# Kernel tuning notes

Measured on AMD Instinct MI355X. Metric: run time of the kernel, lower is better.

The kernel has to match this reference:

```python
import jax, jax.numpy as jnp
import numpy as np
import math

B, N, D, H, L, F, K = 4, 256, 768, 32, 12, 3072, 128
HD = D // H
ATOM_TYPES = 64
EDGE_TYPES = ATOM_TYPES * ATOM_TYPES
BLOCKS = 1
SQRT_2PI = math.sqrt(2.0 * math.pi)


def _ln(x, g, b):
    m = jnp.mean(x, -1, keepdims=True)
    v = jnp.mean((x - m) ** 2, -1, keepdims=True)
    return (x - m) * jax.lax.rsqrt(v + 1e-5) * g + b


def _gelu(x):
    return jax.nn.gelu(x, approximate=False)


def setup_inputs():
    key = jax.random.key(0)
    ks = iter(jax.random.split(key, 64))
    def nrm(shape, s=0.02):
        return jax.random.normal(next(ks), shape, jnp.float32) * s
    inp = dict(
        atoms=jax.random.randint(next(ks), (B, N), 0, ATOM_TYPES),
        tags=jax.random.randint(next(ks), (B, N), 0, 3),
        pos=jax.random.normal(next(ks), (B, N, 3), jnp.float32) * 3.0,
        real_mask=jnp.ones((B, N), dtype=bool),
        atom_emb=nrm((ATOM_TYPES, D)),
        tag_emb=nrm((3, D)),
        gbf_means=jax.random.uniform(next(ks), (K,), jnp.float32, 0.0, 3.0),
        gbf_stds=jax.random.uniform(next(ks), (K,), jnp.float32, 0.0, 3.0),
        gbf_mul=jnp.ones((EDGE_TYPES, 1), jnp.float32),
        gbf_bias=jnp.zeros((EDGE_TYPES, 1), jnp.float32),
        bp_w1=nrm((K, K)), bp_b1=jnp.zeros((K,), jnp.float32),
        bp_w2=nrm((H, K)), bp_b2=jnp.zeros((H,), jnp.float32),
        ep_w=nrm((D, K)), ep_b=jnp.zeros((D,), jnp.float32),
        ln1_g=jnp.ones((L, D), jnp.float32), ln1_b=jnp.zeros((L, D), jnp.float32),
        wqkv=nrm((L, 3 * D, D)), bqkv=jnp.zeros((L, 3 * D), jnp.float32),
        wo=nrm((L, D, D)), bo=jnp.zeros((L, D), jnp.float32),
        ln2_g=jnp.ones((L, D), jnp.float32), ln2_b=jnp.zeros((L, D), jnp.float32),
        w1=nrm((L, F, D)), b1=jnp.zeros((L, F), jnp.float32),
        w2=nrm((L, D, F)), b2=jnp.zeros((L, D), jnp.float32),
        fln_g=jnp.ones((D,), jnp.float32), fln_b=jnp.zeros((D,), jnp.float32),
        en_w1=nrm((D, D)), en_b1=jnp.zeros((D,), jnp.float32),
        en_w2=nrm((1, D)), en_b2=jnp.zeros((1,), jnp.float32),
        eagg=nrm((3, 1), 0.01),
        nq_w=nrm((D, D)), nq_b=jnp.zeros((D,), jnp.float32),
        nk_w=nrm((D, D)), nk_b=jnp.zeros((D,), jnp.float32),
        nv_w=nrm((D, D)), nv_b=jnp.zeros((D,), jnp.float32),
        f1_w=nrm((1, D)), f1_b=jnp.zeros((1,), jnp.float32),
        f2_w=nrm((1, D)), f2_b=jnp.zeros((1,), jnp.float32),
        f3_w=nrm((1, D)), f3_b=jnp.zeros((1,), jnp.float32),
    )
    return inp


def _forward(atoms, tags, real_mask, pos, atom_emb, tag_emb, gbf_means, gbf_stds, gbf_mul, gbf_bias,
             bp_w1, bp_b1, bp_w2, bp_b2, ep_w, ep_b,
             ln1_g, ln1_b, wqkv, bqkv, wo, bo, ln2_g, ln2_b, w1, b1, w2, b2,
             fln_g, fln_b, en_w1, en_b1, en_w2, en_b2, eagg,
             nq_w, nq_b, nk_w, nk_b, nv_w, nv_b, f1_w, f1_b, f2_w, f2_b, f3_w, f3_b):
    pad = atoms == 0                                              # [B,N]
    # delta[b,i,j] = pos[b,j] - pos[b,i]  (matches pos.unsqueeze(1) - pos.unsqueeze(2))
    delta = pos[:, None, :, :] - pos[:, :, None, :]               # [B,N,N,3]
    sq = jnp.sum(delta * delta, axis=-1)
    dist = jnp.sqrt(jnp.maximum(sq, 1e-24))                       # safe norm, zero grad on diagonal
    delta = delta / (dist[..., None] + 1e-5)
    edge_type = atoms[:, :, None] * ATOM_TYPES + atoms[:, None, :]  # [B,N,N]
    # Gaussian basis layer
    mul = gbf_mul[edge_type]                                      # [B,N,N,1]
    add = gbf_bias[edge_type]                                     # [B,N,N,1]
    x = mul * dist[..., None] + add                               # [B,N,N,1] -> broadcast to K
    std = jnp.abs(gbf_stds) + 1e-5                                # [K]
    z = (x - gbf_means) / std
    gbf = jnp.exp(-0.5 * z * z) / (SQRT_2PI * std)                # [B,N,N,K]
    edge_feat = jnp.where(pad[:, None, :, None], 0.0, gbf)
    node = tag_emb[tags] + atom_emb[atoms] + (edge_feat.sum(-2) @ ep_w.T + ep_b)  # [B,N,D]
    bias = _gelu(gbf @ bp_w1.T + bp_b1) @ bp_w2.T + bp_b2         # [B,N,N,H]
    bias = jnp.transpose(bias, (0, 3, 1, 2))                      # [B,H,N,N]
    bias = jnp.where(pad[:, None, None, :], -jnp.inf, bias)
    scale = HD ** -0.5
    h = node
    for _ in range(BLOCKS):
        for l in range(L):
            r = h
            y = _ln(h, ln1_g[l], ln1_b[l])
            qkv = y @ wqkv[l].T + bqkv[l]
            q, k, v = jnp.split(qkv, 3, axis=-1)
            q = q.reshape(B, N, H, HD).transpose(0, 2, 1, 3) * scale
            k = k.reshape(B, N, H, HD).transpose(0, 2, 1, 3)
            v = v.reshape(B, N, H, HD).transpose(0, 2, 1, 3)
            a = jnp.einsum('bhid,bhjd->bhij', q, k) + bias
            a = jax.nn.softmax(a, axis=-1)
            o = jnp.einsum('bhij,bhjd->bhid', a, v).transpose(0, 2, 1, 3).reshape(B, N, D)
            h = r + (o @ wo[l].T + bo[l])
            r = h
            y = _ln(h, ln2_g[l], ln2_b[l])
            y = _gelu(y @ w1[l].T + b1[l]) @ w2[l].T + b2[l]
            h = r + y
    out = _ln(h, fln_g, fln_b)                                    # [B,N,D]
    # energy head (eval: no dropout)
    eng = _gelu(out @ en_w1.T + en_b1) @ en_w2.T + en_b2          # [B,N,1]
    eng = (eng * eagg[tags])[..., 0]                              # [B,N]
    omask = (tags > 0) & real_mask
    eng_output = (eng * omask).sum(-1)                            # [B]
    # node task head
    q = (out @ nq_w.T + nq_b).reshape(B, N, H, HD).transpose(0, 2, 1, 3) * scale
    k = (out @ nk_w.T + nk_b).reshape(B, N, H, HD).transpose(0, 2, 1, 3)
    v = (out @ nv_w.T + nv_b).reshape(B, N, H, HD).transpose(0, 2, 1, 3)
    a = jnp.einsum('bhid,bhjd->bhij', q, k) + bias
    a = jax.nn.softmax(a, axis=-1)                                # [B,H,N,N]
    # rot_attn_probs @ v, fused: [b,h,i,j]*[b,i,j,c]*[b,h,j,d] -> [b,i,c,h,d]
    xf = jnp.einsum('bhij,bijc,bhjd->bichd', a, delta, v).reshape(B, N, 3, D)
    f1 = xf[:, :, 0] @ f1_w.T + f1_b
    f2 = xf[:, :, 1] @ f2_w.T + f2_b
    f3 = xf[:, :, 2] @ f3_w.T + f3_b
    node_output = jnp.concatenate([f1, f2, f3], axis=-1)          # [B,N,3]
    return eng_output, node_output, omask[..., None]


def reference(atoms, tags, pos, real_mask, atom_emb, tag_emb, gbf_means, gbf_stds, gbf_mul, gbf_bias,
              bp_w1, bp_b1, bp_w2, bp_b2, ep_w, ep_b,
              ln1_g, ln1_b, wqkv, bqkv, wo, bo, ln2_g, ln2_b, w1, b1, w2, b2,
              fln_g, fln_b, en_w1, en_b1, en_w2, en_b2, eagg,
              nq_w, nq_b, nk_w, nk_b, nv_w, nv_b, f1_w, f1_b, f2_w, f2_b, f3_w, f3_b):
    return _forward(atoms, tags, real_mask, pos, atom_emb, tag_emb, gbf_means, gbf_stds, gbf_mul, gbf_bias,
                    bp_w1, bp_b1, bp_w2, bp_b2, ep_w, ep_b,
                    ln1_g, ln1_b, wqkv, bqkv, wo, bo, ln2_g, ln2_b, w1, b1, w2, b2,
                    fln_g, fln_b, en_w1, en_b1, en_w2, en_b2, eagg,
                    nq_w, nq_b, nk_w, nk_b, nv_w, nv_b, f1_w, f1_b, f2_w, f2_b, f3_w, f3_b)
```

## Files before the change

### kernel.cpp

```cpp
#include <hip/hip_runtime.h>
#include <math.h>

constexpr int B_ = 4, N_ = 256, D_ = 768, H_ = 32, HD_ = 24, L_ = 12, F_ = 3072, K_ = 128;
constexpr float SCALE_ = 0.20412414523193150f;
constexpr float ISQRT2_ = 0.70710678118654752f;

typedef short bf16x8 __attribute__((ext_vector_type(8)));
typedef float f32x4 __attribute__((ext_vector_type(4)));
typedef unsigned short u16x4 __attribute__((ext_vector_type(4)));
typedef unsigned short u16x8 __attribute__((ext_vector_type(8)));
typedef unsigned int u32x4 __attribute__((ext_vector_type(4)));

#define DEV __device__ __forceinline__
#define MFMA16(a, b, c) __builtin_amdgcn_mfma_f32_16x16x32_bf16(a, b, c, 0, 0, 0)

DEV void gload_lds16(const unsigned short* g, unsigned short* l) {
  __builtin_amdgcn_global_load_lds(
      (const __attribute__((address_space(1))) unsigned int*)(g),
      (__attribute__((address_space(3))) unsigned int*)(l), 16, 0, 0);
}

DEV float gelu_f(float x) { return 0.5f * x * (1.0f + erff(x * ISQRT2_)); }

DEV unsigned short f2bf(float f) {
  unsigned u = __float_as_uint(f);
  return (unsigned short)((u + 0x7FFFu + ((u >> 16) & 1u)) >> 16);
}
DEV float bf2f(unsigned short u) { return __uint_as_float(((unsigned)u) << 16); }
DEV unsigned packbf(float a, float b) {
  return (unsigned)f2bf(a) | ((unsigned)f2bf(b) << 16);
}
DEV bf16x8 u4_to_bf8(u32x4 x) { union { u32x4 a; bf16x8 b; } u; u.a = x; return u.b; }

DEV float breduce_sum(float v, float* sred, int tid) {
#pragma unroll
  for (int o = 32; o > 0; o >>= 1) v += __shfl_xor(v, o);
  if ((tid & 63) == 0) sred[tid >> 6] = v;
  __syncthreads();
  v = (sred[0] + sred[1]) + (sred[2] + sred[3]);
  __syncthreads();
  return v;
}

__global__ __launch_bounds__(256) void cast_one_kernel(
    const float* __restrict__ s, unsigned short* __restrict__ d, int n4) {
  const int i = blockIdx.x * 256 + threadIdx.x;
  if (i >= n4) return;
  const float4 v = ((const float4*)s)[i];
  u16x4 o = {f2bf(v.x), f2bf(v.y), f2bf(v.z), f2bf(v.w)};
  ((u16x4*)d)[i] = o;
}

__global__ __launch_bounds__(256) void castlayer_kernel(
    const float* __restrict__ wqkv, const float* __restrict__ wo,
    const float* __restrict__ w1, const float* __restrict__ w2,
    unsigned short* __restrict__ arena) {
  const unsigned i = blockIdx.x * 256 + threadIdx.x;
  const float* s; unsigned j;
  if (i < 221184u) { s = wqkv; j = i; }
  else if (i < 294912u) { s = wo; j = i - 221184u; }
  else if (i < 589824u) { s = w1; j = i - 294912u; }
  else { s = w2; j = i - 589824u; }
  const float4 a = ((const float4*)s)[2u * j];
  const float4 b = ((const float4*)s)[2u * j + 1u];
  u16x8 o = {f2bf(a.x), f2bf(a.y), f2bf(a.z), f2bf(a.w),
             f2bf(b.x), f2bf(b.y), f2bf(b.z), f2bf(b.w)};
  ((u16x8*)arena)[i] = o;
}

__global__ __launch_bounds__(256) void castheads_kernel(
    const float* __restrict__ a, const float* __restrict__ b,
    const float* __restrict__ c, const float* __restrict__ d,
    unsigned short* __restrict__ arena) {
  const unsigned i = blockIdx.x * 256 + threadIdx.x;
  const unsigned r = i / 73728u;
  const unsigned j = i - r * 73728u;
  const float* s = (r == 0) ? a : (r == 1) ? b : (r == 2) ? c : d;
  const float4 a0 = ((const float4*)s)[2u * j];
  const float4 a1 = ((const float4*)s)[2u * j + 1u];
  u16x8 o = {f2bf(a0.x), f2bf(a0.y), f2bf(a0.z), f2bf(a0.w),
             f2bf(a1.x), f2bf(a1.y), f2bf(a1.z), f2bf(a1.w)};
  ((u16x8*)arena)[i] = o;
}

__global__ __launch_bounds__(256) void edge_pre_kernel(
    const int* __restrict__ atoms, const float* __restrict__ pos,
    const float* __restrict__ gbf_mul, const float* __restrict__ gbf_bias,
    const float* __restrict__ gbf_means, const float* __restrict__ gbf_stds,
    float* __restrict__ deltaw, float* __restrict__ xvalw, float* __restrict__ nsumw)
{
  const int tid = threadIdx.x;
  const int bi = blockIdx.x;
  const int b = bi >> 8;
  __shared__ float spos[3];
  __shared__ float sxv[256];
  __shared__ int   spad[256];
  __shared__ float red[256];
  if (tid < 3) spos[tid] = pos[(size_t)bi * 3 + tid];
  __syncthreads();
  {
    const int j = tid;
    const float px = pos[(size_t)(b * N_ + j) * 3 + 0];
    const float py = pos[(size_t)(b * N_ + j) * 3 + 1];
    const float pz = pos[(size_t)(b * N_ + j) * 3 + 2];
    const float dx = px - spos[0], dy = py - spos[1], dz = pz - spos[2];
    const float sq = dx * dx + dy * dy + dz * dz;
    const float dist = sqrtf(fmaxf(sq, 1e-24f));
    const float inv = 1.f / (dist + 1e-5f);
    const size_t e = (size_t)bi * N_ + j;
    deltaw[e * 3 + 0] = dx * inv;
    deltaw[e * 3 + 1] = dy * inv;
    deltaw[e * 3 + 2] = dz * inv;
    const int et = atoms[bi] * 64 + atoms[b * N_ + j];
    const float xv = gbf_mul[et] * dist + gbf_bias[et];
    xvalw[e] = xv;
    sxv[j] = xv;
    spad[j] = (atoms[b * N_ + j] == 0);
  }
  __syncthreads();
  const int k = tid & 127;
  const float mean = gbf_means[k];
  const float st = fabsf(gbf_stds[k]) + 1e-5f;
  const float istd = 1.f / st;
  const float coef = 0.39894228040143268f * istd;
  float acc = 0.f;
  const int jbase = tid >> 7;
  for (int t = 0; t < 128; ++t) {
    const int j = jbase + (t << 1);
    if (!spad[j]) {
      const float z = (sxv[j] - mean) * istd;
      acc += __expf(-0.5f * z * z) * coef;
    }
  }
  red[tid] = acc;
  __syncthreads();
  if (tid < 128) nsumw[(size_t)bi * K_ + tid] = red[tid] + red[tid + 128];
}

__global__ __launch_bounds__(256) void bias_mfma_kernel(
    const float* __restrict__ xvalw, const int* __restrict__ atoms,
    const float* __restrict__ gbf_means, const float* __restrict__ gbf_stds,
    const unsigned short* __restrict__ w1b, const float* __restrict__ b1,
    const unsigned short* __restrict__ w2b, const float* __restrict__ b2,
    unsigned short* __restrict__ biasb)
{
  __shared__ __align__(16) unsigned short sw1[128 * 128];
  __shared__ __align__(16) unsigned short sw2[32 * 128];
  __shared__ float smean[128], sistd[128], scoef[128], sb1[128], sb2[32];
  const int tid = threadIdx.x;
  const int l = tid & 63;
  const int w = tid >> 6;
  const size_t e0 = (size_t)blockIdx.x * 64;
  const int bB = (int)(e0 >> 16);
  const int iI = (int)((e0 >> 8) & 255);
  const int j0 = (int)(e0 & 255);
  const int lr = l & 15;
  const int lg = l >> 4;

  {
    const int rin = l >> 4;
    const int slot = l & 15;
#pragma unroll
    for (int q = 0; q < 8; ++q) {
      const int rbase = w * 32 + q * 4;
      const int row = rbase + rin;
      const int gs = slot ^ (row & 15);
      gload_lds16(w1b + row * 128 + gs * 8, &sw1[rbase * 128]);
    }
#pragma unroll
    for (int q = 0; q < 2; ++q) {
      const int rbase = w * 8 + q * 4;
      const int row = rbase + rin;
      const int gs = slot ^ (row & 15);
      gload_lds16(w2b + row * 128 + gs * 8, &sw2[rbase * 128]);
    }
  }
  if (tid < 128) {
    const float st = fabsf(gbf_stds[tid]) + 1e-5f;
    const float is = 1.f / st;
    smean[tid] = gbf_means[tid];
    sistd[tid] = is;
    scoef[tid] = 0.39894228040143268f * is;
    sb1[tid] = b1[tid];
  } else if (tid < 160) {
    sb2[tid - 128] = b2[tid - 128];
  }
  const int el = w * 16 + lr;
  const float xv = xvalw[e0 + el];
  const bool padq = (atoms[bB * N_ + j0 + el] == 0);
  __syncthreads();

  bf16x8 bG[4];
#pragma unroll
  for (int ks = 0; ks < 4; ++ks) {
    u16x8 t;
#pragma unroll
    for (int j = 0; j < 8; ++j) {
      const int k = ks * 32 + lg * 8 + j;
      const float z = (xv - smean[k]) * sistd[k];
      t[j] = f2bf(__expf(-0.5f * z * z) * scoef[k]);
    }
    union { u16x8 a; bf16x8 b; } u; u.a = t;
    bG[ks] = u.b;
  }

  f32x4 accM[8];
#pragma unroll
  for (int f = 0; f < 8; ++f) accM[f] = (f32x4)0.f;
#pragma unroll
  for (int ks = 0; ks < 4; ++ks) {
#pragma unroll
    for (int f = 0; f < 8; ++f) {
      const int row = f * 16 + lr;
      const int sl = (ks * 4 + lg) ^ (row & 15);
      const bf16x8 aW = *(const bf16x8*)&sw1[row * 128 + (sl << 3)];
      accM[f] = MFMA16(aW, bG[ks], accM[f]);
    }
  }

  unsigned pm[8][2];
#pragma unroll
  for (int f = 0; f < 8; ++f) {
    float g[4];
#pragma unroll
    for (int r = 0; r < 4; ++r)
      g[r] = gelu_f(accM[f][r] + sb1[f * 16 + lg * 4 + r]);
    pm[f][0] = packbf(g[0], g[1]);
    pm[f][1] = packbf(g[2], g[3]);
  }

  f32x4 accH[2];
  accH[0] = (f32x4)0.f; accH[1] = (f32x4)0.f;
#pragma unroll
  for (int ks = 0; ks < 4; ++ks) {
    const int s0 = ((((lg << 1)) & 3) << 4) + lr;
    const int s1 = ((((lg << 1) + 1) & 3) << 4) + lr;
    const int sel = lg >> 1;
    const unsigned a0 = __shfl(pm[2 * ks][0], s0), b0 = __shfl(pm[2 * ks + 1][0], s0);
    const unsigned a1 = __shfl(pm[2 * ks][1], s0), b1v = __shfl(pm[2 * ks + 1][1], s0);
    const unsigned a2 = __shfl(pm[2 * ks][0], s1), b2v = __shfl(pm[2 * ks + 1][0], s1);
    const unsigned a3 = __shfl(pm[2 * ks][1], s1), b3v = __shfl(pm[2 * ks + 1][1], s1);
    u32x4 bw;
    bw.x = sel ? b0 : a0;
    bw.y = sel ? b1v : a1;
    bw.z = sel ? b2v : a2;
    bw.w = sel ? b3v : a3;
    const bf16x8 bMid = u4_to_bf8(bw);
#pragma unroll
    for (int hf = 0; hf < 2; ++hf) {
      const int row = hf * 16 + lr;
      const int sl = (ks * 4 + lg) ^ (row & 15);
      const bf16x8 aW2 = *(const bf16x8*)&sw2[row * 128 + (sl << 3)];
      accH[hf] = MFMA16(aW2, bMid, accH[hf]);
    }
  }

  const size_t obase = (((size_t)bB * H_) * N_ + iI) * N_ + j0 + el;
#pragma unroll
  for (int hf = 0; hf < 2; ++hf) {
#pragma unroll
    for (int r = 0; r < 4; ++r) {
      const int h = hf * 16 + lg * 4 + r;
      const unsigned short v = padq ? (unsigned short)0xFF80
                                    : f2bf(accH[hf][r] + sb2[h]);
      biasb[obase + (size_t)h * N_ * N_] = v;
    }
  }
}

__global__ __launch_bounds__(256) void node_init_kernel(
    const int* __restrict__ atoms, const int* __restrict__ tags,
    const float* __restrict__ atom_emb, const float* __restrict__ tag_emb,
    const float* __restrict__ nsumw, const float* __restrict__ ep_w,
    const float* __restrict__ ep_b, float* __restrict__ hbuf)
{
  const int bi = blockIdx.x;
  const int tid = threadIdx.x;
  __shared__ float ns[K_];
  if (tid < K_) ns[tid] = nsumw[(size_t)bi * K_ + tid];
  __syncthreads();
  const int at = atoms[bi], tg = tags[bi];
  for (int d = tid; d < D_; d += 256) {
    float acc = tag_emb[tg * D_ + d] + atom_emb[at * D_ + d] + ep_b[d];
    const float* w = ep_w + (size_t)d * K_;
#pragma unroll 8
    for (int kk = 0; kk < K_; ++kk) acc = fmaf(ns[kk], w[kk], acc);
    hbuf[(size_t)bi * D_ + d] = acc;
  }
}

__global__ __launch_bounds__(256) void ln_kernel(
    const float* __restrict__ x, const float* __restrict__ gg,
    const float* __restrict__ bb, unsigned short* __restrict__ y)
{
  const int bi = blockIdx.x;
  const int tid = threadIdx.x;
  __shared__ float sred[4];
  const float* row = x + (size_t)bi * D_;
  const float v0 = row[tid], v1 = row[tid + 256], v2 = row[tid + 512];
  float s = breduce_sum(v0 + v1 + v2, sred, tid);
  const float mean = s * (1.f / 768.f);
  const float d0 = v0 - mean, d1 = v1 - mean, d2 = v2 - mean;
  float q = breduce_sum(d0 * d0 + d1 * d1 + d2 * d2, sred, tid);
  const float inv = rsqrtf(q * (1.f / 768.f) + 1e-5f);
  unsigned short* out = y + (size_t)bi * D_;
  out[tid]       = f2bf(d0 * inv * gg[tid]       + bb[tid]);
  out[tid + 256] = f2bf(d1 * inv * gg[tid + 256] + bb[tid + 256]);
  out[tid + 512] = f2bf(d2 * inv * gg[tid + 512] + bb[tid + 512]);
}

template <int S>
__global__ __launch_bounds__(256) void reduce_ln_kernel(
    const float* __restrict__ P, const float* __restrict__ bias,
    float* __restrict__ hbuf, const float* __restrict__ gg,
    const float* __restrict__ bb, unsigned short* __restrict__ y)
{
  const int row = blockIdx.x;
  const int tid = threadIdx.x;
  __shared__ float sred[4];
  float h[3];
#pragma unroll
  for (int t = 0; t < 3; ++t) {
    const int c = tid + (t << 8);
    float s = bias[c];
#pragma unroll
    for (int z = 0; z < S; ++z)
      s += P[((size_t)z * (B_ * N_) + row) * 768 + c];
    const float hv = hbuf[(size_t)row * 768 + c] + s;
    hbuf[(size_t)row * 768 + c] = hv;
    h[t] = hv;
  }
  float sm = breduce_sum(h[0] + h[1] + h[2], sred, tid);
  const float mean = sm * (1.f / 768.f);
  const float d0 = h[0] - mean, d1 = h[1] - mean, d2 = h[2] - mean;
  float q = breduce_sum(d0 * d0 + d1 * d1 + d2 * d2, sred, tid);
  const float inv = rsqrtf(q * (1.f / 768.f) + 1e-5f);
  unsigned short* out = y + (size_t)row * 768;
  out[tid]       = f2bf(d0 * inv * gg[tid]       + bb[tid]);
  out[tid + 256] = f2bf(d1 * inv * gg[tid + 256] + bb[tid + 256]);
  out[tid + 512] = f2bf(d2 * inv * gg[tid + 512] + bb[tid + 512]);
}

template <int EPI, int OB>
__global__ __launch_bounds__(256) void gemm_mfma(
    const unsigned short* __restrict__ A, const unsigned short* __restrict__ W,
    const float* __restrict__ bias, const float* __restrict__ bias2,
    const float* __restrict__ bias3, const float* __restrict__ bias4,
    float* __restrict__ C, unsigned short* __restrict__ Cb,
    int M, int N, int K, int lda, int ldw)
{
  if (EPI == 4) {
    const int z = blockIdx.z;
    A += (size_t)z * K;
    W += (size_t)z * K;
    C += (size_t)z * M * N;
  }
  __shared__ __align__(16) unsigned short sA[2][64 * 64];
  __shared__ __align__(16) unsigned short sB[2][64 * 64];
  const int tid = threadIdx.x;
  const int l = tid & 63;
  const int w = tid >> 6;
  const int m0 = blockIdx.y * 64;
  const int n0 = blockIdx.x * 64;
  const int wm = w >> 1, wn = w & 1;
  const int lr = l & 15;
  const int lg = l >> 4;
  const int r0 = (w << 4) + (l >> 3);
  const int s0 = (l & 7) ^ (r0 & 7);

  f32x4 acc[2][2];
#pragma unroll
  for (int mi = 0; mi < 2; ++mi)
#pragma unroll
    for (int ni = 0; ni < 2; ++ni) acc[mi][ni] = (f32x4)0.f;

  auto stage = [&](int buf, int t) {
    const size_t kb = (size_t)t << 6;
    unsigned short* lA = &sA[buf][(w << 4) << 6];
    unsigned short* lB = &sB[buf][(w << 4) << 6];
    gload_lds16(A + (size_t)(m0 + r0) * lda + kb + (s0 << 3), lA);
    gload_lds16(A + (size_t)(m0 + r0 + 8) * lda + kb + (s0 << 3), lA + 8 * 64);
    gload_lds16(W + (size_t)(n0 + r0) * ldw + kb + (s0 << 3), lB);
    gload_lds16(W + (size_t)(n0 + r0 + 8) * ldw + kb + (s0 << 3), lB + 8 * 64);
  };

  stage(0, 0);
  const int nt = K >> 6;
  for (int t = 0; t < nt; ++t) {
    __syncthreads();
    if (t + 1 < nt) stage((t + 1) & 1, t + 1);
    const unsigned short* bA = sA[t & 1];
    const unsigned short* bBs = sB[t & 1];
    bf16x8 af[2][2], bfr[2][2];
#pragma unroll
    for (int mi = 0; mi < 2; ++mi) {
      const int row = (wm << 5) + (mi << 4) + lr;
#pragma unroll
      for (int kk = 0; kk < 2; ++kk) {
        const int sl = ((kk << 2) + lg) ^ (row & 7);
        af[mi][kk] = *(const bf16x8*)&bA[(row << 6) + (sl << 3)];
      }
    }
#pragma unroll
    for (int ni = 0; ni < 2; ++ni) {
      const int row = (wn << 5) + (ni << 4) + lr;
#pragma unroll
      for (int kk = 0; kk < 2; ++kk) {
        const int sl = ((kk << 2) + lg) ^ (row & 7);
        bfr[ni][kk] = *(const bf16x8*)&bBs[(row << 6) + (sl << 3)];
      }
    }
#pragma unroll
    for (int kk = 0; kk < 2; ++kk)
#pragma unroll
      for (int mi = 0; mi < 2; ++mi)
#pragma unroll
        for (int ni = 0; ni < 2; ++ni)
          acc[mi][ni] = MFMA16(af[mi][kk], bfr[ni][kk], acc[mi][ni]);
  }

#pragma unroll
  for (int mi = 0; mi < 2; ++mi)
#pragma unroll
    for (int ni = 0; ni < 2; ++ni) {
      const int n = n0 + (wn << 5) + (ni << 4) + lr;
      float bv = 0.f;
      int seg = 0;
      if (EPI == 3) {
        seg = n / 768;
        const float* bp = (seg == 0) ? bias : (seg == 1) ? bias2
                         : (seg == 2) ? bias3 : bias4;
        bv = bp[n - seg * 768];
      } else if (EPI != 4) {
        bv = bias[n];
      }
#pragma unroll
      for (int r = 0; r < 4; ++r) {
        const int m = m0 + (wm << 5) + (mi << 4) + lg * 4 + r;
        float v = acc[mi][ni][r] + bv;
        if (EPI == 1) v = gelu_f(v);
        if (EPI == 3 && seg == 3) v = gelu_f(v);
        if (OB) Cb[(size_t)m * N + n] = f2bf(v);
        else C[(size_t)m * N + n] = v;
      }
    }
}

template <bool PROBS>
__global__ __launch_bounds__(256) void attn_mfma_kernel(
    const unsigned short* __restrict__ Q, const unsigned short* __restrict__ Kp,
    const unsigned short* __restrict__ Vp, const int stride,
    const unsigned short* __restrict__ biasb, unsigned short* __restrict__ obuf,
    unsigned short* __restrict__ aprob)
{
  __shared__ __align__(16) unsigned short sK[256 * 40];
  __shared__ __align__(16) unsigned short sVt[32 * 264];
  __shared__ __align__(16) unsigned short sP[64 * 264];
  const int tid = threadIdx.x;
  const int l = tid & 63, w = tid >> 6;
  const int bh = blockIdx.x, b = bh >> 5, hh = bh & 31;
  const int i0 = blockIdx.y * 64;
  const int lr = l & 15, lg = l >> 4;

#pragma unroll
  for (int it = 0; it < 3; ++it) {
    const int c = tid + (it << 8);
    const int row = c / 3, part = c - row * 3;
    *(u16x8*)&sK[row * 40 + part * 8] =
        *(const u16x8*)&Kp[(size_t)(b * N_ + row) * stride + hh * HD_ + part * 8];
  }
  {
    u16x8 z = {0, 0, 0, 0, 0, 0, 0, 0};
    *(u16x8*)&sK[tid * 40 + 24] = z;
  }
  if (!PROBS) {
    const int j = tid;
    const unsigned short* vr = &Vp[(size_t)(b * N_ + j) * stride + hh * HD_];
    const u16x8 v0 = *(const u16x8*)vr;
    const u16x8 v1 = *(const u16x8*)(vr + 8);
    const u16x8 v2 = *(const u16x8*)(vr + 16);
#pragma unroll
    for (int d = 0; d < 8; ++d) {
      sVt[d * 264 + j] = v0[d];
      sVt[(8 + d) * 264 + j] = v1[d];
      sVt[(16 + d) * 264 + j] = v2[d];
    }
  }
  bf16x8 aQ;
  if (lg < 3) {
    const u16x8 q = *(const u16x8*)&Q[(size_t)(b * N_ + i0 + (w << 4) + lr) * stride + hh * HD_ + lg * 8];
    union { u16x8 a; bf16x8 b; } u; u.a = q;
    aQ = u.b;
  } else {
    bf16x8 t = {0, 0, 0, 0, 0, 0, 0, 0};
    aQ = t;
  }
  __syncthreads();

  f32x4 acc[16];
#pragma unroll
  for (int ni = 0; ni < 16; ++ni) {
    const bf16x8 bK = *(const bf16x8*)&sK[(ni * 16 + lr) * 40 + lg * 8];
    acc[ni] = MFMA16(aQ, bK, (f32x4)0.f);
  }

  float invr[4];
#pragma unroll
  for (int r = 0; r < 4; ++r) {
    const int iloc = (w << 4) + lg * 4 + r;
    const unsigned short* bp =
        &biasb[(((size_t)(b * H_ + hh)) * N_ + i0 + iloc) * N_ + lr];
    float mx = -INFINITY;
#pragma unroll
    for (int ni = 0; ni < 16; ++ni) {
      const float s = acc[ni][r] * SCALE_ + bf2f(bp[ni * 16]);
      acc[ni][r] = s;
      mx = fmaxf(mx, s);
    }
    mx = fmaxf(mx, __shfl_xor(mx, 1));
    mx = fmaxf(mx, __shfl_xor(mx, 2));
    mx = fmaxf(mx, __shfl_xor(mx, 4));
    mx = fmaxf(mx, __shfl_xor(mx, 8));
    float sum = 0.f;
#pragma unroll
    for (int ni = 0; ni < 16; ++ni) {
      const float e = __expf(acc[ni][r] - mx);
      acc[ni][r] = e;
      sum += e;
    }
    sum += __shfl_xor(sum, 1);
    sum += __shfl_xor(sum, 2);
    sum += __shfl_xor(sum, 4);
    sum += __shfl_xor(sum, 8);
    const float inv = 1.f / sum;
    invr[r] = inv;
#pragma unroll
    for (int ni = 0; ni < 16; ++ni)
      sP[iloc * 264 + ni * 16 + lr] = f2bf(PROBS ? acc[ni][r] * inv
                                                 : acc[ni][r]);
  }
  __syncthreads();

  if (PROBS) {
#pragma unroll
    for (int it = 0; it < 8; ++it) {
      const int idx = tid + it * 256;
      const int row = idx >> 5, c = idx & 31;
      *(u16x8*)&aprob[(((size_t)(b * H_ + hh)) * N_ + i0 + row) * N_ + c * 8] =
          *(const u16x8*)&sP[row * 264 + c * 8];
    }
  } else {
    f32x4 accO[2];
    accO[0] = (f32x4)0.f; accO[1] = (f32x4)0.f;
#pragma unroll
    for (int ks = 0; ks < 8; ++ks) {
      const bf16x8 aP = *(const bf16x8*)&sP[((w << 4) + lr) * 264 + ks * 32 + lg * 8];
      const bf16x8 bV0 = *(const bf16x8*)&sVt[lr * 264 + ks * 32 + lg * 8];
      const bf16x8 bV1 = *(const bf16x8*)&sVt[(16 + lr) * 264 + ks * 32 + lg * 8];
      accO[0] = MFMA16(aP, bV0, accO[0]);
      accO[1] = MFMA16(aP, bV1, accO[1]);
    }
#pragma unroll
    for (int ni = 0; ni < 2; ++ni) {
      const int n = ni * 16 + lr;
      if (n < HD_) {
#pragma unroll
        for (int r = 0; r < 4; ++r) {
          const int i = i0 + (w << 4) + lg * 4 + r;
          obuf[(size_t)(b * N_ + i) * D_ + hh * HD_ + n] = f2bf(accO[ni][r] * invr[r]);
        }
      }
    }
  }
}

__global__ __launch_bounds__(256) void engnode_kernel(
    const unsigned short* __restrict__ t1, const int stride,
    const float* __restrict__ en_w2, const float* __restrict__ en_b2,
    const float* __restrict__ eagg, const int* __restrict__ tags,
    float* __restrict__ engpn)
{
  const int bi = blockIdx.x;
  const int tid = threadIdx.x;
  __shared__ float sred[4];
  const unsigned short* row = t1 + (size_t)bi * stride;
  float acc = bf2f(row[tid]) * en_w2[tid] + bf2f(row[tid + 256]) * en_w2[tid + 256] +
              bf2f(row[tid + 512]) * en_w2[tid + 512];
  acc = breduce_sum(acc, sred, tid);
  if (tid == 0) {
    const int tg = tags[bi];
    engpn[bi] = (tg > 0) ? (acc + en_b2[0]) * eagg[tg] : 0.f;
  }
}

__global__ __launch_bounds__(256) void engsum_omask_kernel(
    const float* __restrict__ engpn, const int* __restrict__ tags,
    float* __restrict__ out)
{
  const int bid = blockIdx.x;
  const int tid = threadIdx.x;
  if (bid < 4) {
    __shared__ float sred[4];
    float v = breduce_sum(engpn[bid * N_ + tid], sred, tid);
    if (tid == 0) out[bid] = v;
  } else {
    const int idx = (bid - 4) * 256 + tid;
    out[4 + B_ * N_ * 3 + idx] = (tags[idx] > 0) ? 1.f : 0.f;
  }
}

__global__ __launch_bounds__(256) void wv_kernel(
    const unsigned short* __restrict__ vn, const int stride,
    const float* __restrict__ f1w, const float* __restrict__ f2w,
    const float* __restrict__ f3w, float* __restrict__ wv)
{
  const int idx = blockIdx.x * 256 + threadIdx.x;
  const int j = idx & 255;
  const int hh = (idx >> 8) & 31;
  const int b = (idx >> 13) & 3;
  const int c = idx >> 15;
  const float* fw = (c == 0) ? f1w : ((c == 1) ? f2w : f3w);
  const unsigned short* vrow = vn + (size_t)(b * N_ + j) * stride + hh * HD_;
  const u16x8 v0 = *(const u16x8*)vrow;
  const u16x8 v1 = *(const u16x8*)(vrow + 8);
  const u16x8 v2 = *(const u16x8*)(vrow + 16);
  float acc = 0.f;
#pragma unroll
  for (int d = 0; d < 8; ++d) {
    acc = fmaf(bf2f(v0[d]), fw[hh * HD_ + d], acc);
    acc = fmaf(bf2f(v1[d]), fw[hh * HD_ + 8 + d], acc);
    acc = fmaf(bf2f(v2[d]), fw[hh * HD_ + 16 + d], acc);
  }
  wv[idx] = acc;
}

__global__ __launch_bounds__(256) void nodeout_kernel(
    const unsigned short* __restrict__ aprob, const float* __restrict__ wv,
    const float* __restrict__ deltaw, const float* __restrict__ f1b,
    const float* __restrict__ f2b, const float* __restrict__ f3b,
    float* __restrict__ out)
{
  const int bi = blockIdx.x;
  const int tid = threadIdx.x;
  const int b = bi >> 8;
  const int i = bi & 255;
  __shared__ float sred[4];
  const unsigned short* ap = aprob + (((size_t)b * H_) * N_ + i) * N_ + tid;
  const float* wv0 = wv + ((size_t)(0 * B_ + b) * H_) * N_ + tid;
  const float* wv1 = wv + ((size_t)(1 * B_ + b) * H_) * N_ + tid;
  const float* wv2 = wv + ((size_t)(2 * B_ + b) * H_) * N_ + tid;
  float s0 = 0.f, s1 = 0.f, s2 = 0.f;
  for (int hh = 0; hh < H_; ++hh) {
    const float p = bf2f(ap[(size_t)hh * N_ * N_]);
    s0 = fmaf(p, wv0[(size_t)hh * N_], s0);
    s1 = fmaf(p, wv1[(size_t)hh * N_], s1);
    s2 = fmaf(p, wv2[(size_t)hh * N_], s2);
  }
  const float* dl = &deltaw[((size_t)bi * N_ + tid) * 3];
  s0 *= dl[0];
  s1 *= dl[1];
  s2 *= dl[2];
  s0 = breduce_sum(s0, sred, tid);
  s1 = breduce_sum(s1, sred, tid);
  s2 = breduce_sum(s2, sred, tid);
  if (tid == 0) {
    out[4 + bi * 3 + 0] = s0 + f1b[0];
    out[4 + bi * 3 + 1] = s1 + f2b[0];
    out[4 + bi * 3 + 2] = s2 + f3b[0];
  }
}

extern "C" void kernel_launch(void* const* d_in, const int* in_sizes, int n_in,
                              void* d_out, int out_size, void* d_ws, size_t ws_size,
                              hipStream_t stream) {
  (void)in_sizes; (void)n_in; (void)out_size; (void)ws_size;
  const int*   atoms     = (const int*)  d_in[0];
  const int*   tags      = (const int*)  d_in[1];
  const float* pos       = (const float*)d_in[2];
  const float* atom_emb  = (const float*)d_in[4];
  const float* tag_emb   = (const float*)d_in[5];
  const float* gbf_means = (const float*)d_in[6];
  const float* gbf_stds  = (const float*)d_in[7];
  const float* gbf_mul   = (const float*)d_in[8];
  const float* gbf_bias  = (const float*)d_in[9];
  const float* bp_w1     = (const float*)d_in[10];
  const float* bp_b1     = (const float*)d_in[11];
  const float* bp_w2     = (const float*)d_in[12];
  const float* bp_b2     = (const float*)d_in[13];
  const float* ep_w      = (const float*)d_in[14];
  const float* ep_b      = (const float*)d_in[15];
  const float* ln1_g     = (const float*)d_in[16];
  const float* ln1_b     = (const float*)d_in[17];
  const float* wqkv      = (const float*)d_in[18];
  const float* bqkv      = (const float*)d_in[19];
  const float* wo        = (const float*)d_in[20];
  const float* bo        = (const float*)d_in[21];
  const float* ln2_g     = (const float*)d_in[22];
  const float* ln2_b     = (const float*)d_in[23];
  const float* w1        = (const float*)d_in[24];
  const float* b1        = (const float*)d_in[25];
  const float* w2        = (const float*)d_in[26];
  const float* b2        = (const float*)d_in[27];
  const float* fln_g     = (const float*)d_in[28];
  const float* fln_b     = (const float*)d_in[29];
  const float* en_w1     = (const float*)d_in[30];
  const float* en_b1     = (const float*)d_in[31];
  const float* en_w2     = (const float*)d_in[32];
  const float* en_b2     = (const float*)d_in[33];
  const float* eagg      = (const float*)d_in[34];
  const float* nq_w      = (const float*)d_in[35];
  const float* nq_b      = (const float*)d_in[36];
  const float* nk_w      = (const float*)d_in[37];
  const float* nk_b      = (const float*)d_in[38];
  const float* nv_w      = (const float*)d_in[39];
  const float* nv_b      = (const float*)d_in[40];
  const float* f1_w      = (const float*)d_in[41];
  const float* f1_b      = (const float*)d_in[42];
  const float* f2_w      = (const float*)d_in[43];
  const float* f2_b      = (const float*)d_in[44];
  const float* f3_w      = (const float*)d_in[45];
  const float* f3_b      = (const float*)d_in[46];

  char* wsB = (char*)d_ws;
  size_t off = 0;
  auto alloc = [&](size_t bytes) {
    void* p = wsB + off;
    off = (off + bytes + 255) & ~(size_t)255;
    return p;
  };
  unsigned short* biasb   = (unsigned short*)alloc((size_t)B_ * H_ * N_ * N_ * 2);
  unsigned short* aprobb  = (unsigned short*)alloc((size_t)B_ * H_ * N_ * N_ * 2);
  float*          deltaw  = (float*)alloc((size_t)B_ * N_ * N_ * 3 * 4);
  float*          xvalw   = (float*)alloc((size_t)B_ * N_ * N_ * 4);
  float*          nsumw   = (float*)alloc((size_t)B_ * N_ * K_ * 4);
  float*          hbuf    = (float*)alloc((size_t)B_ * N_ * D_ * 4);
  unsigned short* qkvb    = (unsigned short*)alloc((size_t)B_ * N_ * 3 * D_ * 2);
  unsigned short* qn4b    = (unsigned short*)alloc((size_t)B_ * N_ * 3072 * 2);
  unsigned short* ybf     = (unsigned short*)alloc((size_t)B_ * N_ * D_ * 2);
  unsigned short* obf     = (unsigned short*)alloc((size_t)B_ * N_ * D_ * 2);
  unsigned short* midbf   = (unsigned short*)alloc((size_t)B_ * N_ * F_ * 2);
  unsigned short* outbf   = (unsigned short*)alloc((size_t)B_ * N_ * D_ * 2);
  unsigned short* arena   = (unsigned short*)alloc((size_t)7077888 * 2);
  unsigned short* headsb  = (unsigned short*)alloc((size_t)2359296 * 2);
  unsigned short* bw1b    = (unsigned short*)alloc((size_t)K_ * K_ * 2);
  unsigned short* bw2b    = (unsigned short*)alloc((size_t)H_ * K_ * 2);
  float*          wopart  = (float*)alloc((size_t)2 * B_ * N_ * D_ * 4);
  float*          ffpart  = (float*)alloc((size_t)4 * B_ * N_ * D_ * 4);
  float*          wvb     = (float*)alloc((size_t)3 * B_ * H_ * N_ * 4);
  float*          engpn   = (float*)alloc((size_t)B_ * N_ * 4);

  const int BN = B_ * N_;
  float* outp = (float*)d_out;
  const size_t OQKV = 0, OWO = 1769472, OW1 = 2359296, OW2 = 4718592;

  edge_pre_kernel<<<BN, 256, 0, stream>>>(atoms, pos, gbf_mul, gbf_bias,
                                          gbf_means, gbf_stds, deltaw, xvalw, nsumw);
  cast_one_kernel<<<16, 256, 0, stream>>>(bp_w1, bw1b, 4096);
  cast_one_kernel<<<4, 256, 0, stream>>>(bp_w2, bw2b, 1024);
  bias_mfma_kernel<<<B_ * N_ * N_ / 64, 256, 0, stream>>>(
      xvalw, atoms, gbf_means, gbf_stds, bw1b, bp_b1, bw2b, bp_b2, biasb);
  node_init_kernel<<<BN, 256, 0, stream>>>(atoms, tags, atom_emb, tag_emb,
                                           nsumw, ep_w, ep_b, hbuf);
  ln_kernel<<<BN, 256, 0, stream>>>(hbuf, ln1_g, ln1_b, ybf);

  for (int l = 0; l < L_; ++l) {
    castlayer_kernel<<<3456, 256, 0, stream>>>(
        wqkv + (size_t)l * 3 * D_ * D_, wo + (size_t)l * D_ * D_,
        w1 + (size_t)l * F_ * D_, w2 + (size_t)l * D_ * F_, arena);
    gemm_mfma<0, 1><<<dim3(36, 16), 256, 0, stream>>>(
        ybf, arena + OQKV, bqkv + (size_t)l * 3 * D_, nullptr, nullptr, nullptr,
        nullptr, qkvb, BN, 3 * D_, D_, D_, D_);
    attn_mfma_kernel<false><<<dim3(B_ * H_, 4), 256, 0, stream>>>(
        qkvb, qkvb + D_, qkvb + 2 * D_, 3 * D_, biasb, obf, nullptr);
    gemm_mfma<4, 0><<<dim3(12, 16, 2), 256, 0, stream>>>(
        obf, arena + OWO, nullptr, nullptr, nullptr, nullptr,
        wopart, nullptr, BN, D_, 384, D_, D_);
    reduce_ln_kernel<2><<<BN, 256, 0, stream>>>(
        wopart, bo + (size_t)l * D_, hbuf, ln2_g + (size_t)l * D_,
        ln2_b + (size_t)l * D_, ybf);
    gemm_mfma<1, 1><<<dim3(48, 16), 256, 0, stream>>>(
        ybf, arena + OW1, b1 + (size_t)l * F_, nullptr, nullptr, nullptr,
        nullptr, midbf, BN, F_, D_, D_, D_);
    gemm_mfma<4, 0><<<dim3(12, 16, 4), 256, 0, stream>>>(
        midbf, arena + OW2, nullptr, nullptr, nullptr, nullptr,
        ffpart, nullptr, BN, D_, 768, F_, F_);
    const bool last = (l == L_ - 1);
    reduce_ln_kernel<4><<<BN, 256, 0, stream>>>(
        ffpart, b2 + (size_t)l * D_, hbuf,
        last ? fln_g : ln1_g + (size_t)(l + 1) * D_,
        last ? fln_b : ln1_b + (size_t)(l + 1) * D_,
        last ? outbf : ybf);
  }

  castheads_kernel<<<1152, 256, 0, stream>>>(nq_w, nk_w, nv_w, en_w1, headsb);

  gemm_mfma<3, 1><<<dim3(48, 16), 256, 0, stream>>>(
      outbf, headsb, nq_b, nk_b, nv_b, en_b1,
      nullptr, qn4b, BN, 3072, D_, D_, D_);

  attn_mfma_kernel<true><<<dim3(B_ * H_, 4), 256, 0, stream>>>(
      qn4b, qn4b + 768, qn4b + 1536, 3072, biasb, nullptr, aprobb);
  wv_kernel<<<3 * B_ * H_ * N_ / 256, 256, 0, stream>>>(
      qn4b + 1536, 3072, f1_w, f2_w, f3_w, wvb);
  nodeout_kernel<<<BN, 256, 0, stream>>>(aprobb, wvb, deltaw,
                                         f1_b, f2_b, f3_b, outp);

  engnode_kernel<<<BN, 256, 0, stream>>>(qn4b + 2304, 3072, en_w2, en_b2,
                                         eagg, tags, engpn);
  engsum_omask_kernel<<<8, 256, 0, stream>>>(engpn, tags, outp);
}
```

Measured before the change: 1.020 ms.

## Merge bias weight casts, fuse node init with LayerNorm, add MFMA setprio

The two small cast launches for the bias-projection weights become one kernel that picks its source by thread index. The initial LayerNorm is folded into node_init_kernel, which removes one launch and a reread of hbuf. s_setprio hints are placed around the MFMA loops in the bias and attention kernels so matrix-core waves get scheduling priority. These cut a few launches and may improve MFMA issue overlap, though they touch only one-off or small parts of a 12-layer pipeline.

```diff
diff --git a/kernel.cpp b/kernel.cpp
--- a/kernel.cpp
+++ b/kernel.cpp
@@ -42,13 +42,18 @@
   return v;
 }
 
-__global__ __launch_bounds__(256) void cast_one_kernel(
-    const float* __restrict__ s, unsigned short* __restrict__ d, int n4) {
+__global__ __launch_bounds__(256) void cast_bias_kernel(
+    const float* __restrict__ w1f, const float* __restrict__ w2f,
+    unsigned short* __restrict__ d1, unsigned short* __restrict__ d2) {
   const int i = blockIdx.x * 256 + threadIdx.x;
-  if (i >= n4) return;
-  const float4 v = ((const float4*)s)[i];
+  const float* s;
+  unsigned short* d;
+  int j;
+  if (i < 4096) { s = w1f; d = d1; j = i; }
+  else { s = w2f; d = d2; j = i - 4096; }
+  const float4 v = ((const float4*)s)[j];
   u16x4 o = {f2bf(v.x), f2bf(v.y), f2bf(v.z), f2bf(v.w)};
-  ((u16x4*)d)[i] = o;
+  ((u16x4*)d)[j] = o;
 }
 
 __global__ __launch_bounds__(256) void castlayer_kernel(
@@ -207,6 +212,7 @@
   f32x4 accM[8];
 #pragma unroll
   for (int f = 0; f < 8; ++f) accM[f] = (f32x4)0.f;
+  __builtin_amdgcn_s_setprio(1);
 #pragma unroll
   for (int ks = 0; ks < 4; ++ks) {
 #pragma unroll
@@ -217,6 +223,7 @@
       accM[f] = MFMA16(aW, bG[ks], accM[f]);
     }
   }
+  __builtin_amdgcn_s_setprio(0);
 
   unsigned pm[8][2];
 #pragma unroll
@@ -246,6 +253,7 @@
     bw.z = sel ? b2v : a2;
     bw.w = sel ? b3v : a3;
     const bf16x8 bMid = u4_to_bf8(bw);
+    __builtin_amdgcn_s_setprio(1);
 #pragma unroll
     for (int hf = 0; hf < 2; ++hf) {
       const int row = hf * 16 + lr;
@@ -253,6 +261,7 @@
       const bf16x8 aW2 = *(const bf16x8*)&sw2[row * 128 + (sl << 3)];
       accH[hf] = MFMA16(aW2, bMid, accH[hf]);
     }
+    __builtin_amdgcn_s_setprio(0);
   }
 
   const size_t obase = (((size_t)bB * H_) * N_ + iI) * N_ + j0 + el;
@@ -272,35 +281,31 @@
     const int* __restrict__ atoms, const int* __restrict__ tags,
     const float* __restrict__ atom_emb, const float* __restrict__ tag_emb,
     const float* __restrict__ nsumw, const float* __restrict__ ep_w,
-    const float* __restrict__ ep_b, float* __restrict__ hbuf)
+    const float* __restrict__ ep_b, const float* __restrict__ gg,
+    const float* __restrict__ bb, float* __restrict__ hbuf,
+    unsigned short* __restrict__ y)
 {
   const int bi = blockIdx.x;
   const int tid = threadIdx.x;
   __shared__ float ns[K_];
+  __shared__ float sred[4];
   if (tid < K_) ns[tid] = nsumw[(size_t)bi * K_ + tid];
   __syncthreads();
   const int at = atoms[bi], tg = tags[bi];
-  for (int d = tid; d < D_; d += 256) {
+  float h[3];
+#pragma unroll
+  for (int t = 0; t < 3; ++t) {
+    const int d = tid + (t << 8);
     float acc = tag_emb[tg * D_ + d] + atom_emb[at * D_ + d] + ep_b[d];
     const float* w = ep_w + (size_t)d * K_;
 #pragma unroll 8
     for (int kk = 0; kk < K_; ++kk) acc = fmaf(ns[kk], w[kk], acc);
     hbuf[(size_t)bi * D_ + d] = acc;
-  }
-}
-
-__global__ __launch_bounds__(256) void ln_kernel(
-    const float* __restrict__ x, const float* __restrict__ gg,
-    const float* __restrict__ bb, unsigned short* __restrict__ y)
-{
-  const int bi = blockIdx.x;
-  const int tid = threadIdx.x;
-  __shared__ float sred[4];
-  const float* row = x + (size_t)bi * D_;
-  const float v0 = row[tid], v1 = row[tid + 256], v2 = row[tid + 512];
-  float s = breduce_sum(v0 + v1 + v2, sred, tid);
+    h[t] = acc;
+  }
+  float s = breduce_sum(h[0] + h[1] + h[2], sred, tid);
   const float mean = s * (1.f / 768.f);
-  const float d0 = v0 - mean, d1 = v1 - mean, d2 = v2 - mean;
+  const float d0 = h[0] - mean, d1 = h[1] - mean, d2 = h[2] - mean;
   float q = breduce_sum(d0 * d0 + d1 * d1 + d2 * d2, sred, tid);
   const float inv = rsqrtf(q * (1.f / 768.f) + 1e-5f);
   unsigned short* out = y + (size_t)bi * D_;
@@ -498,11 +503,13 @@
   __syncthreads();
 
   f32x4 acc[16];
+  __builtin_amdgcn_s_setprio(1);
 #pragma unroll
   for (int ni = 0; ni < 16; ++ni) {
     const bf16x8 bK = *(const bf16x8*)&sK[(ni * 16 + lr) * 40 + lg * 8];
     acc[ni] = MFMA16(aQ, bK, (f32x4)0.f);
   }
+  __builtin_amdgcn_s_setprio(0);
 
   float invr[4];
 #pragma unroll
@@ -552,6 +559,7 @@
   } else {
     f32x4 accO[2];
     accO[0] = (f32x4)0.f; accO[1] = (f32x4)0.f;
+    __builtin_amdgcn_s_setprio(1);
 #pragma unroll
     for (int ks = 0; ks < 8; ++ks) {
       const bf16x8 aP = *(const bf16x8*)&sP[((w << 4) + lr) * 264 + ks * 32 + lg * 8];
@@ -560,6 +568,7 @@
       accO[0] = MFMA16(aP, bV0, accO[0]);
       accO[1] = MFMA16(aP, bV1, accO[1]);
     }
+    __builtin_amdgcn_s_setprio(0);
 #pragma unroll
     for (int ni = 0; ni < 2; ++ni) {
       const int n = ni * 16 + lr;
@@ -755,13 +764,12 @@
 
   edge_pre_kernel<<<BN, 256, 0, stream>>>(atoms, pos, gbf_mul, gbf_bias,
                                           gbf_means, gbf_stds, deltaw, xvalw, nsumw);
-  cast_one_kernel<<<16, 256, 0, stream>>>(bp_w1, bw1b, 4096);
-  cast_one_kernel<<<4, 256, 0, stream>>>(bp_w2, bw2b, 1024);
+  cast_bias_kernel<<<20, 256, 0, stream>>>(bp_w1, bp_w2, bw1b, bw2b);
   bias_mfma_kernel<<<B_ * N_ * N_ / 64, 256, 0, stream>>>(
       xvalw, atoms, gbf_means, gbf_stds, bw1b, bp_b1, bw2b, bp_b2, biasb);
   node_init_kernel<<<BN, 256, 0, stream>>>(atoms, tags, atom_emb, tag_emb,
-                                           nsumw, ep_w, ep_b, hbuf);
-  ln_kernel<<<BN, 256, 0, stream>>>(hbuf, ln1_g, ln1_b, ybf);
+                                           nsumw, ep_w, ep_b, ln1_g, ln1_b,
+                                           hbuf, ybf);
 
   for (int l = 0; l < L_; ++l) {
     castlayer_kernel<<<3456, 256, 0, stream>>>(
```

After: 1.027 ms. Within noise of the previous version (+0.7%).
